# Optimization experiments

Hardware: AMD Instinct MI355X
Metric: run time of the kernel (lower is better)

Reference implementation:

```python
import jax, jax.numpy as jnp
import numpy as np

LN_EPS = 1e-5

def _layer_norm(x, g, b):
    mu = jnp.mean(x, axis=-1, keepdims=True)
    var = jnp.mean(jnp.square(x - mu), axis=-1, keepdims=True)
    return (x - mu) * jax.lax.rsqrt(var + LN_EPS) * g + b

def setup_inputs() -> dict:
    key = jax.random.key(0)
    ks = jax.random.split(key, 12)
    B, L, E, H, W = 4, 1024, 1024, 16, 128
    s = 0.02
    return {
        "x": jax.random.normal(ks[0], (B, L, E), dtype=jnp.float32),
        "in_proj_w": jax.random.normal(ks[1], (3 * E, E), dtype=jnp.float32) * s,
        "in_proj_b": jnp.zeros((3 * E,), dtype=jnp.float32),
        "out_proj_w": jax.random.normal(ks[2], (E, E), dtype=jnp.float32) * s,
        "out_proj_b": jnp.zeros((E,), dtype=jnp.float32),
        "ln1_g": jnp.ones((E,), dtype=jnp.float32),
        "ln1_b": jnp.zeros((E,), dtype=jnp.float32),
        "w1": jax.random.normal(ks[3], (4 * E, E), dtype=jnp.float32) * s,
        "b1": jnp.zeros((4 * E,), dtype=jnp.float32),
        "w2": jax.random.normal(ks[4], (E, 4 * E), dtype=jnp.float32) * s,
        "b2": jnp.zeros((E,), dtype=jnp.float32),
        "ln2_g": jnp.ones((E,), dtype=jnp.float32),
        "ln2_b": jnp.zeros((E,), dtype=jnp.float32),
        "n_head": 16,
        "window_size": 128,
    }

def reference(x, in_proj_w, in_proj_b, out_proj_w, out_proj_b,
              ln1_g, ln1_b, w1, b1, w2, b2, ln2_g, ln2_b,
              n_head, window_size):
    B, L, E = x.shape
    H = n_head
    D = E // H
    # qkv projection (torch Linear convention: y = x @ W.T + b)
    qkv = jnp.einsum('ble,fe->blf', x, in_proj_w) + in_proj_b  # [B,L,3E]
    q, k, v = jnp.split(qkv, 3, axis=-1)
    q = q.reshape(B, L, H, D).transpose(0, 2, 1, 3)  # [B,H,L,D]
    k = k.reshape(B, L, H, D).transpose(0, 2, 1, 3)
    v = v.reshape(B, L, H, D).transpose(0, 2, 1, 3)
    scores = jnp.einsum('bhld,bhmd->bhlm', q, k) / np.sqrt(D)  # [B,H,L,L]
    # banded window mask: allowed iff |i-j| <= window_size (same as the double loop)
    idx = jnp.arange(L)
    band = jnp.abs(idx[:, None] - idx[None, :]) <= window_size  # [L,L]
    scores = jnp.where(band[None, None], scores, -jnp.inf)
    attn = jax.nn.softmax(scores, axis=-1)  # [B,H,L,L]
    ctx = jnp.einsum('bhlm,bhmd->bhld', attn, v)  # [B,H,L,D]
    ctx = ctx.transpose(0, 2, 1, 3).reshape(B, L, E)
    attn_out = jnp.einsum('ble,fe->blf', ctx, out_proj_w) + out_proj_b
    attn_weights = jnp.mean(attn, axis=1)  # torch MHA averages heads -> [B,L,L]
    # residual + norm1 (dropout is identity in eval)
    h = _layer_norm(x + attn_out, ln1_g, ln1_b)
    # positionwise FFN
    ff = jnp.einsum('ble,fe->blf', h, w1) + b1
    ff = jax.nn.relu(ff)
    ff = jnp.einsum('blf,ef->ble', ff, w2) + b2
    out = _layer_norm(h + ff, ln2_g, ln2_b)
    return (out, attn_weights)
```

## Files before the change

### kernel.cpp

```cpp
#include <hip/hip_runtime.h>

#define BB 4
#define LL 1024
#define EE 1024
#define HH 16
#define DD 64

typedef __attribute__((ext_vector_type(8))) short short8;
typedef __attribute__((ext_vector_type(4))) float floatx4;

#define PSTR ((size_t)4096 * 1024)

__device__ __forceinline__ float bf2f(short s) {
    union { unsigned u; float f; } c;
    c.u = ((unsigned)(unsigned short)s) << 16;
    return c.f;
}
__device__ __forceinline__ short f2bf(float f) {
    union { float f; unsigned u; } c; c.f = f;
    unsigned r = c.u + 0x7fffu + ((c.u >> 16) & 1u);
    return (short)(r >> 16);
}

__device__ __forceinline__ void async_copy16(const void* g, void* l) {
    __builtin_amdgcn_global_load_lds(
        (const __attribute__((address_space(1))) unsigned int*)g,
        (__attribute__((address_space(3))) unsigned int*)l, 16, 0, 0);
}

__global__ __launch_bounds__(256) void cvt5(
    const float* __restrict__ x, const float* __restrict__ wqkv,
    const float* __restrict__ wo, const float* __restrict__ w1,
    const float* __restrict__ w2,
    short* __restrict__ xb, short* __restrict__ wqkvb, short* __restrict__ wob,
    short* __restrict__ w1b, short* __restrict__ w2b)
{
    int bi = blockIdx.x;
    const float* in; short* out; int base;
    if      (bi <  4096) { in = x;    out = xb;    base = 0;     }
    else if (bi <  7168) { in = wqkv; out = wqkvb; base = 4096;  }
    else if (bi <  8192) { in = wo;   out = wob;   base = 7168;  }
    else if (bi < 12288) { in = w1;   out = w1b;   base = 8192;  }
    else                 { in = w2;   out = w2b;   base = 12288; }
    int i = (bi - base) * 256 + threadIdx.x;
    float4 v = ((const float4*)in)[i];
    unsigned long long u =
          (unsigned long long)(unsigned short)f2bf(v.x)
        | ((unsigned long long)(unsigned short)f2bf(v.y) << 16)
        | ((unsigned long long)(unsigned short)f2bf(v.z) << 32)
        | ((unsigned long long)(unsigned short)f2bf(v.w) << 48);
    ((unsigned long long*)out)[i] = u;
}

template<bool RELU, bool SK>
__global__ __launch_bounds__(512, 2) void gemm256(
    const short* __restrict__ A, const short* __restrict__ Bw,
    const float* __restrict__ bias,
    short* __restrict__ Cb,
    int M, int N, int K, int Ksp)
{
    __shared__ short SH[67584];
    const int tid  = threadIdx.x;
    const int w    = tid >> 6, lane = tid & 63;
    const int fr   = lane & 15, quad = lane >> 4;
    const int wm   = w >> 2,  wn   = w & 3;

    const int gx   = gridDim.x;
    const int flat = blockIdx.y * gx + blockIdx.x;
    const int nwg  = gx * gridDim.y;
    const int q8   = nwg >> 3;
    const int swz  = (flat & 7) * q8 + (flat >> 3);
    const int m0   = (swz % gx) * 256;
    const int n0   = (swz / gx) * 256;

    const int kb = SK ? blockIdx.z * Ksp : 0;
    const int NT = (SK ? Ksp : K) >> 5;

    auto stageA = [&](int s) {
        if (s >= NT) return;
#pragma unroll
        for (int l = 0; l < 2; ++l) {
            int r = l * 128 + (tid >> 2);
            int g = (tid & 3) ^ ((r >> 1) & 3);
            async_copy16(A + (size_t)(m0 + r) * K + kb + s * 32 + g * 8,
                         SH + (s & 3) * 16384 + l * 4096 + w * 512);
        }
    };
    auto stageB = [&](int s) {
        if (s >= NT) return;
#pragma unroll
        for (int l = 0; l < 2; ++l) {
            int r = l * 128 + (tid >> 2);
            int g = (tid & 3) ^ ((r >> 1) & 3);
            async_copy16(Bw + (size_t)(n0 + r) * K + kb + s * 32 + g * 8,
                         SH + (s & 3) * 16384 + 8192 + l * 4096 + w * 512);
        }
    };

    floatx4 acc[8][4];
#pragma unroll
    for (int i = 0; i < 8; ++i)
#pragma unroll
        for (int j = 0; j < 4; ++j) acc[i][j] = (floatx4){0.f, 0.f, 0.f, 0.f};

    stageA(0); stageB(0); stageA(1); stageB(1); stageA(2); stageB(2);

    const int pos = (quad ^ ((fr >> 1) & 3)) * 8;

    for (int t = 0; t < NT; ++t) {
        if (t + 2 < NT)      asm volatile("s_waitcnt vmcnt(8)" ::: "memory");
        else if (t + 1 < NT) asm volatile("s_waitcnt vmcnt(4)" ::: "memory");
        else                 asm volatile("s_waitcnt vmcnt(0)" ::: "memory");
        __builtin_amdgcn_sched_barrier(0);
        __builtin_amdgcn_s_barrier();
        __builtin_amdgcn_sched_barrier(0);

        const short* sA = SH + (t & 3) * 16384;
        const short* sB = sA + 8192;

        stageA(t + 3);

        short8 af[8], bf[4];
#pragma unroll
        for (int i = 0; i < 4; ++i) af[i] = *(const short8*)&sA[(wm * 128 + i * 16 + fr) * 32 + pos];
#pragma unroll
        for (int j = 0; j < 4; ++j) bf[j] = *(const short8*)&sB[(wn * 64 + j * 16 + fr) * 32 + pos];

        __builtin_amdgcn_s_setprio(1);
#pragma unroll
        for (int i = 0; i < 4; ++i)
#pragma unroll
            for (int j = 0; j < 4; ++j)
                acc[i][j] = __builtin_amdgcn_mfma_f32_16x16x32_bf16(af[i], bf[j], acc[i][j], 0, 0, 0);
        __builtin_amdgcn_s_setprio(0);

        stageB(t + 3);
#pragma unroll
        for (int i = 0; i < 4; ++i) af[i + 4] = *(const short8*)&sA[(wm * 128 + (i + 4) * 16 + fr) * 32 + pos];

        __builtin_amdgcn_s_setprio(1);
#pragma unroll
        for (int i = 0; i < 4; ++i)
#pragma unroll
            for (int j = 0; j < 4; ++j)
                acc[i + 4][j] = __builtin_amdgcn_mfma_f32_16x16x32_bf16(af[i + 4], bf[j], acc[i + 4][j], 0, 0, 0);
        __builtin_amdgcn_s_setprio(0);
        __builtin_amdgcn_sched_barrier(0);
    }

    __syncthreads();

    const int cc = lane & 15, rb4 = quad * 4;
#pragma unroll
    for (int i = 0; i < 8; ++i) {
        int row = wm * 128 + i * 16 + rb4;
#pragma unroll
        for (int j = 0; j < 4; ++j) {
            int col = wn * 64 + j * 16 + cc;
            float bv = SK ? 0.0f : bias[n0 + col];
#pragma unroll
            for (int r = 0; r < 4; ++r) {
                float v = acc[i][j][r] + bv;
                if (RELU) v = fmaxf(v, 0.0f);
                SH[(row + r) * 264 + col] = f2bf(v);
            }
        }
    }
    __syncthreads();
    short* Co = Cb + (SK ? (size_t)blockIdx.z * PSTR : 0);
#pragma unroll
    for (int it = 0; it < 16; ++it) {
        int idx = it * 512 + tid;
        int row = idx >> 5, ch = idx & 31;
        short8 v = *(const short8*)&SH[row * 264 + ch * 8];
        *(short8*)&Co[(size_t)(m0 + row) * N + n0 + ch * 8] = v;
    }
}

__global__ __launch_bounds__(256) void vtrans(const short* __restrict__ qkv,
                                              short* __restrict__ vt)
{
    int id = blockIdx.x;
    int tb = id & 15, h = (id >> 4) & 15, b = id >> 8;
    __shared__ short T[64 * 72];
    const short* src = qkv + (size_t)(b * 1024 + tb * 64) * 3072 + 2048 + h * 64;
    int tok = threadIdx.x >> 2;
    int c8  = threadIdx.x & 3;
#pragma unroll
    for (int q = 0; q < 2; ++q) {
        int d0 = (c8 * 2 + q) * 8;
        short8 v = *(const short8*)&src[(size_t)tok * 3072 + d0];
#pragma unroll
        for (int e = 0; e < 8; ++e) T[(d0 + e) * 72 + tok] = v[e];
    }
    __syncthreads();
    short* dst = vt + (size_t)((b * 16 + h) * 64) * 1024 + tb * 64;
    int d = threadIdx.x >> 2, cq = threadIdx.x & 3;
#pragma unroll
    for (int q = 0; q < 2; ++q) {
        int t0 = (cq * 2 + q) * 8;
        *(short8*)&dst[(size_t)d * 1024 + t0] = *(const short8*)&T[d * 72 + t0];
    }
}

template<bool RELU, bool SK>
__global__ __launch_bounds__(256) void gemm_bt(
    const short* __restrict__ A, const short* __restrict__ Bw,
    const float* __restrict__ bias,
    short* __restrict__ Cb,
    int M, int N, int K, int Ksp)
{
    __shared__ union U {
        struct { short As[128 * 64]; short Bs[128 * 64]; } s;
        short Cs[128 * 136];
    } u;
    const int tid  = threadIdx.x;
    const int wave = tid >> 6, lane = tid & 63;
    const int m0 = blockIdx.x * 128, n0 = blockIdx.y * 128;
    const int wm = (wave & 1) * 64, wn = (wave >> 1) * 64;
    const int kbase = SK ? blockIdx.z * Ksp : 0;

    floatx4 acc[4][4];
#pragma unroll
    for (int i = 0; i < 4; ++i)
#pragma unroll
        for (int j = 0; j < 4; ++j) acc[i][j] = (floatx4){0.f, 0.f, 0.f, 0.f};

    const int srow = wave * 8 + (lane >> 3);
    const int scol = (((lane & 7) ^ ((lane >> 3) & 7))) * 8;
    const short* gA = A  + (size_t)(m0 + srow) * K + kbase + scol;
    const short* gB = Bw + (size_t)(n0 + srow) * K + kbase + scol;
    short* lA = u.s.As + wave * 512;
    short* lB = u.s.Bs + wave * 512;

    const int fr = lane & 15, quad = lane >> 4;
    const int kiters = (SK ? Ksp : K) >> 6;
    for (int kt = 0; kt < kiters; ++kt) {
#pragma unroll
        for (int s = 0; s < 4; ++s) {
            async_copy16(gA + (size_t)s * 32 * K, lA + s * 2048);
            async_copy16(gB + (size_t)s * 32 * K, lB + s * 2048);
        }
        gA += 64; gB += 64;
        __syncthreads();
#pragma unroll
        for (int ks = 0; ks < 2; ++ks) {
            short8 af[4], bf[4];
#pragma unroll
            for (int i = 0; i < 4; ++i) {
                int pos = ((ks * 4 + quad) ^ (fr & 7)) * 8;
                af[i] = *(const short8*)&u.s.As[(wm + i * 16 + fr) * 64 + pos];
                bf[i] = *(const short8*)&u.s.Bs[(wn + i * 16 + fr) * 64 + pos];
            }
#pragma unroll
            for (int i = 0; i < 4; ++i)
#pragma unroll
                for (int j = 0; j < 4; ++j)
                    acc[i][j] = __builtin_amdgcn_mfma_f32_16x16x32_bf16(af[i], bf[j], acc[i][j], 0, 0, 0);
        }
        __syncthreads();
    }

    const int cc = lane & 15;
    const int rb = (lane >> 4) * 4;
#pragma unroll
    for (int j = 0; j < 4; ++j) {
        int col = wn + j * 16 + cc;
        float bv = SK ? 0.0f : bias[n0 + col];
#pragma unroll
        for (int i = 0; i < 4; ++i) {
            int row = wm + i * 16 + rb;
#pragma unroll
            for (int r = 0; r < 4; ++r) {
                float v = acc[i][j][r] + bv;
                if (RELU) v = fmaxf(v, 0.0f);
                u.Cs[(row + r) * 136 + col] = f2bf(v);
            }
        }
    }
    __syncthreads();
    short* Co = Cb + (SK ? (size_t)blockIdx.z * PSTR : 0);
    const int trow = tid >> 4, tcol = (tid & 15) * 8;
#pragma unroll
    for (int p = 0; p < 8; ++p) {
        int row = p * 16 + trow;
        short8 vv = *(const short8*)&u.Cs[row * 136 + tcol];
        *(short8*)&Co[(size_t)(m0 + row) * N + n0 + tcol] = vv;
    }
}

__global__ __launch_bounds__(256) void ln_kernel(
    const float* __restrict__ xa, const short* __restrict__ parts, int nparts,
    const float* __restrict__ bias,
    const float* __restrict__ g, const float* __restrict__ beta,
    float* __restrict__ outf, short* __restrict__ outb)
{
    const int row = blockIdx.x;
    const int tid = threadIdx.x;
    float4 va = ((const float4*)(xa + (size_t)row * EE))[tid];
    float4 vb = ((const float4*)bias)[tid];
    float v0 = va.x + vb.x, v1 = va.y + vb.y, v2 = va.z + vb.z, v3 = va.w + vb.w;
#pragma unroll 4
    for (int p = 0; p < nparts; ++p) {
        unsigned long long u8 = ((const unsigned long long*)(parts + p * PSTR + (size_t)row * EE))[tid];
        v0 += bf2f((short)(u8 & 0xffff));
        v1 += bf2f((short)((u8 >> 16) & 0xffff));
        v2 += bf2f((short)((u8 >> 32) & 0xffff));
        v3 += bf2f((short)(u8 >> 48));
    }
    float s  = v0 + v1 + v2 + v3;
    float ss = v0 * v0 + v1 * v1 + v2 * v2 + v3 * v3;
#pragma unroll
    for (int o = 1; o < 64; o <<= 1) { s += __shfl_xor(s, o); ss += __shfl_xor(ss, o); }
    __shared__ float red[8];
    if ((tid & 63) == 0) { red[(tid >> 6) * 2] = s; red[(tid >> 6) * 2 + 1] = ss; }
    __syncthreads();
    s  = red[0] + red[2] + red[4] + red[6];
    ss = red[1] + red[3] + red[5] + red[7];
    float mean = s * (1.0f / EE);
    float var  = ss * (1.0f / EE) - mean * mean;
    float rstd = rsqrtf(var + 1e-5f);
    float4 vg = ((const float4*)g)[tid];
    float4 vt = ((const float4*)beta)[tid];
    float o0 = (v0 - mean) * rstd * vg.x + vt.x;
    float o1 = (v1 - mean) * rstd * vg.y + vt.y;
    float o2 = (v2 - mean) * rstd * vg.z + vt.z;
    float o3 = (v3 - mean) * rstd * vg.w + vt.w;
    if (outf) ((float4*)(outf + (size_t)row * EE))[tid] = make_float4(o0, o1, o2, o3);
    if (outb) {
        unsigned long long u =
              (unsigned long long)(unsigned short)f2bf(o0)
            | ((unsigned long long)(unsigned short)f2bf(o1) << 16)
            | ((unsigned long long)(unsigned short)f2bf(o2) << 32)
            | ((unsigned long long)(unsigned short)f2bf(o3) << 48);
        ((unsigned long long*)(outb + (size_t)row * EE))[tid] = u;
    }
}

__global__ __launch_bounds__(512, 4) void attn_mfma(
    const short* __restrict__ qkv,
    const short* __restrict__ vt,
    short* __restrict__ ctxp,
    short* __restrict__ pb)
{
    __shared__ short Kl[64 * 320];
    __shared__ float Red[2][2][64];
    const int tid = threadIdx.x, w = tid >> 6, lane = tid & 63;
    const int quad = lane >> 4, mcol = lane & 15;
    const int id = blockIdx.x;
    const int i0 = (id >> 6) * 64, h = id & 15, b = (id >> 4) & 3;
    const int jb0 = i0 - 128;

    const short* qb = qkv + (size_t)(b * 1024) * 3072 + h * 64;
    const short* kb = qb + 1024;

    {
        short* dstb = Kl + w * 512;
#pragma unroll
        for (int it = 0; it < 5; ++it) {
            int jo = it * 64 + w * 8 + (lane >> 3);
            int j  = min(max(jb0 + jo, 0), 1023);
            int g  = (lane & 7) ^ (jo & 7);
            async_copy16(kb + (size_t)j * 3072 + g * 8, dstb + it * 4096);
        }
    }

    const int mt = w >> 1, qtr = w & 1;
    const short* qrow = qb + (size_t)(i0 + mt * 16 + mcol) * 3072 + quad * 8;
    short8 aq0 = *(const short8*)qrow;
    short8 aq1 = *(const short8*)(qrow + 32);

    __syncthreads();

    floatx4 sacc[10];
#pragma unroll
    for (int c = 0; c < 10; ++c) sacc[c] = (floatx4){0.f, 0.f, 0.f, 0.f};
#pragma unroll
    for (int c = 0; c < 10; ++c) {
        int jo = qtr * 160 + c * 16 + mcol;
        const short* krow = Kl + jo * 64;
        short8 b0 = *(const short8*)&krow[((quad    ) ^ (jo & 7)) * 8];
        short8 b1 = *(const short8*)&krow[((4 + quad) ^ (jo & 7)) * 8];
        sacc[c] = __builtin_amdgcn_mfma_f32_16x16x32_bf16(aq0, b0, sacc[c], 0, 0, 0);
        sacc[c] = __builtin_amdgcn_mfma_f32_16x16x32_bf16(aq1, b1, sacc[c], 0, 0, 0);
    }

    const int row0 = mt * 16 + quad * 4;
#pragma unroll
    for (int r = 0; r < 4; ++r) {
        int row = row0 + r;
        float m = -1e30f;
#pragma unroll
        for (int c = 0; c < 10; ++c) {
            int jo = qtr * 160 + c * 16 + mcol;
            bool val = (jo >= row) && (jo <= row + 256) && ((unsigned)(jb0 + jo) < 1024u);
            float s = val ? sacc[c][r] * 0.125f : -1e30f;
            sacc[c][r] = s;
            m = fmaxf(m, s);
        }
        m = fmaxf(m, __shfl_xor(m, 1));
        m = fmaxf(m, __shfl_xor(m, 2));
        m = fmaxf(m, __shfl_xor(m, 4));
        m = fmaxf(m, __shfl_xor(m, 8));
        if (mcol == 0) Red[qtr][0][row] = m;
    }
    __syncthreads();
#pragma unroll
    for (int r = 0; r < 4; ++r) {
        int row = row0 + r;
        float M = fmaxf(Red[0][0][row], Red[1][0][row]);
        float l = 0.f;
#pragma unroll
        for (int c = 0; c < 10; ++c) {
            float p = __expf(sacc[c][r] - M);
            sacc[c][r] = p;
            l += p;
        }
        l += __shfl_xor(l, 1);
        l += __shfl_xor(l, 2);
        l += __shfl_xor(l, 4);
        l += __shfl_xor(l, 8);
        if (mcol == 0) Red[qtr][1][row] = l;
    }
    __syncthreads();
    short* Pl = Kl;
#pragma unroll
    for (int r = 0; r < 4; ++r) {
        int row = row0 + r;
        float inv = 1.0f / (Red[0][1][row] + Red[1][1][row]);
#pragma unroll
        for (int c = 0; c < 10; ++c) {
            int jo = qtr * 160 + c * 16 + mcol;
            Pl[row * 320 + (((jo >> 3) ^ (row & 7)) * 8) + (jo & 7)] = f2bf(sacc[c][r] * inv);
        }
    }
    __syncthreads();

    const int pmt = w & 3, dth = w >> 2;
    floatx4 cacc[2];
    cacc[0] = (floatx4){0.f, 0.f, 0.f, 0.f};
    cacc[1] = (floatx4){0.f, 0.f, 0.f, 0.f};
    const int prow = (pmt * 16 + mcol) * 320;
    const short* vb0 = vt + ((size_t)((b * 16 + h) * 64 + dth * 32) + mcol) * 1024;
#pragma unroll
    for (int jc = 0; jc < 10; ++jc) {
        short8 ap = *(const short8*)&Pl[prow + (((jc * 4 + quad) ^ (mcol & 7)) * 8)];
        int jg = jb0 + jc * 32 + quad * 8;
        if ((unsigned)jg >= 1024u) jg = 0;
        short8 bv0 = *(const short8*)(vb0 + jg);
        short8 bv1 = *(const short8*)(vb0 + (size_t)16 * 1024 + jg);
        cacc[0] = __builtin_amdgcn_mfma_f32_16x16x32_bf16(ap, bv0, cacc[0], 0, 0, 0);
        cacc[1] = __builtin_amdgcn_mfma_f32_16x16x32_bf16(ap, bv1, cacc[1], 0, 0, 0);
    }

    short* pbb = pb + ((size_t)((b * 16 + h) * 1024) + i0) * 320;
#pragma unroll
    for (int s = 0; s < 5; ++s) {
        int t = s * 512 + tid;
        int row = t / 40, c = t - row * 40;
        short8 v = *(const short8*)&Pl[row * 320 + ((c ^ (row & 7)) * 8)];
        *(short8*)&pbb[(size_t)t * 8] = v;
    }
    __syncthreads();

    short* Ct = Kl;
#pragma unroll
    for (int d2 = 0; d2 < 2; ++d2)
#pragma unroll
        for (int r = 0; r < 4; ++r)
            Ct[(pmt * 16 + quad * 4 + r) * 72 + dth * 32 + d2 * 16 + mcol] = f2bf(cacc[d2][r]);
    __syncthreads();
    short* cb = ctxp + (size_t)(b * 1024 + i0) * 1024 + h * 64;
    {
        int row = tid >> 3, c = tid & 7;
        short8 v = *(const short8*)&Ct[row * 72 + c * 8];
        *(short8*)&cb[(size_t)row * 1024 + c * 8] = v;
    }
}

__global__ __launch_bounds__(256) void pb_reduce(const short* __restrict__ pb,
                                                 float* __restrict__ aw)
{
    const int i = blockIdx.x & 1023, b = blockIdx.x >> 10;
    const int i0 = i & ~63;
    __shared__ short P[16 * 320];
    for (int t = threadIdx.x; t < 640; t += 256) {
        int hh = t / 40, c = t - hh * 40;
        ((short8*)P)[t] = *(const short8*)(pb +
            ((size_t)((b * 16 + hh) * 1024) + i) * 320 + c * 8);
    }
    __syncthreads();
    float* row = aw + ((size_t)(b * 1024) + i) * 1024;
    for (int j = threadIdx.x; j < 1024; j += 256) {
        int jo = j - i0 + 128;
        float s = 0.f;
        if ((unsigned)jo < 320u) {
#pragma unroll
            for (int hh = 0; hh < 16; ++hh)
                s += bf2f(P[hh * 320 + jo]);
            s *= (1.0f / 16.0f);
        }
        row[j] = s;
    }
}

extern "C" void kernel_launch(void* const* d_in, const int* in_sizes, int n_in,
                              void* d_out, int out_size, void* d_ws, size_t ws_size,
                              hipStream_t stream) {
    const float* x    = (const float*)d_in[0];
    const float* wqkv = (const float*)d_in[1];
    const float* bqkv = (const float*)d_in[2];
    const float* wo   = (const float*)d_in[3];
    const float* bo   = (const float*)d_in[4];
    const float* g1   = (const float*)d_in[5];
    const float* be1  = (const float*)d_in[6];
    const float* w1   = (const float*)d_in[7];
    const float* bb1  = (const float*)d_in[8];
    const float* w2   = (const float*)d_in[9];
    const float* bb2  = (const float*)d_in[10];
    const float* g2   = (const float*)d_in[11];
    const float* be2  = (const float*)d_in[12];

    char* ws = (char*)d_ws;
    size_t off = 0;
    auto take = [&](size_t bytes) {
        void* p = ws + off;
        off += (bytes + 255) & ~(size_t)255;
        return p;
    };
    short* xb     = (short*)take((size_t)4096 * 1024 * 2);
    short* wqkv_b = (short*)take((size_t)3072 * 1024 * 2);
    short* wo_b   = (short*)take((size_t)1024 * 1024 * 2);
    short* w1_b   = (short*)take((size_t)4096 * 1024 * 2);
    short* w2_b   = (short*)take((size_t)1024 * 4096 * 2);
    short* qkv_b  = (short*)take((size_t)4096 * 3072 * 2);
    short* ctx_b  = (short*)take((size_t)4096 * 1024 * 2);
    short* ff2_p  = qkv_b;
    short* attn_p = (short*)take((size_t)2 * 4096 * 1024 * 2);
    float* h_f    = (float*)take((size_t)4096 * 1024 * 4);
    short* vt_ws  = (short*)h_f;
    short* h_b    = (short*)take((size_t)4096 * 1024 * 2);
    short* pb_ws  = (short*)take((size_t)4 * 16 * 1024 * 320 * 2);
    short* ff_b   = pb_ws;

    float* out_f = (float*)d_out;
    float* attnW = (float*)d_out + (size_t)4 * 1024 * 1024;

    cvt5<<<16384, 256, 0, stream>>>(x, wqkv, wo, w1, w2, xb, wqkv_b, wo_b, w1_b, w2_b);

    gemm256<false, false><<<dim3(16, 12), 512, 0, stream>>>(
        xb, wqkv_b, bqkv, qkv_b, 4096, 3072, 1024, 1024);

    vtrans<<<1024, 256, 0, stream>>>(qkv_b, vt_ws);

    attn_mfma<<<1024, 512, 0, stream>>>(qkv_b, vt_ws, ctx_b, pb_ws);

    pb_reduce<<<4096, 256, 0, stream>>>(pb_ws, attnW);

    gemm_bt<false, true><<<dim3(32, 8, 2), 256, 0, stream>>>(
        ctx_b, wo_b, nullptr, attn_p, 4096, 1024, 1024, 512);

    ln_kernel<<<4096, 256, 0, stream>>>(x, attn_p, 2, bo, g1, be1, h_f, h_b);

    gemm256<true, false><<<dim3(16, 16), 512, 0, stream>>>(
        h_b, w1_b, bb1, ff_b, 4096, 4096, 1024, 1024);

    gemm256<false, true><<<dim3(16, 4, 4), 512, 0, stream>>>(
        ff_b, w2_b, nullptr, ff2_p, 4096, 1024, 4096, 1024);

    ln_kernel<<<4096, 256, 0, stream>>>(h_f, ff2_p, 4, bb2, g2, be2, out_f, nullptr);
}
```

Before: 332.9 us.

## Switch GEMM mainloop to K=64 tiles with two-stage double buffering

The bf16 MFMA GEMM mainloop now processes 64-wide K tiles instead of 32, using two LDS buffers with a single `__syncthreads` per step in place of a four-stage ring with hand-tuned `vmcnt` waits. The A and B staging are merged into one lambda with an 8-way XOR swizzle suited to the wider rows, and each iteration issues two K-halves of 32 MFMAs. This halves the number of barriers per K and lets more MFMAs run per sync. The trade-off is that prefetch depth drops from three tiles ahead to one, so global-load latency may be hidden less well.

```diff
diff --git a/kernel.cpp b/kernel.cpp
--- a/kernel.cpp
+++ b/kernel.cpp
@@ -74,28 +74,27 @@
     const int n0   = (swz / gx) * 256;
 
     const int kb = SK ? blockIdx.z * Ksp : 0;
-    const int NT = (SK ? Ksp : K) >> 5;
-
-    auto stageA = [&](int s) {
+    const int NT = (SK ? Ksp : K) >> 6;
+
+    const int srow = w * 8 + (lane >> 3);
+    const int sg   = lane & 7;
+    auto stage = [&](int s) {
         if (s >= NT) return;
 #pragma unroll
-        for (int l = 0; l < 2; ++l) {
-            int r = l * 128 + (tid >> 2);
-            int g = (tid & 3) ^ ((r >> 1) & 3);
-            async_copy16(A + (size_t)(m0 + r) * K + kb + s * 32 + g * 8,
-                         SH + (s & 3) * 16384 + l * 4096 + w * 512);
+        for (int i = 0; i < 4; ++i) {
+            int r = i * 64 + srow;
+            int g = sg ^ (r & 7);
+            async_copy16(A + (size_t)(m0 + r) * K + kb + s * 64 + g * 8,
+                         SH + (s & 1) * 32768 + i * 4096 + w * 512);
+        }
+#pragma unroll
+        for (int i = 0; i < 4; ++i) {
+            int r = i * 64 + srow;
+            int g = sg ^ (r & 7);
+            async_copy16(Bw + (size_t)(n0 + r) * K + kb + s * 64 + g * 8,
+                         SH + (s & 1) * 32768 + 16384 + i * 4096 + w * 512);
         }
     };
-    auto stageB = [&](int s) {
-        if (s >= NT) return;
-#pragma unroll
-        for (int l = 0; l < 2; ++l) {
-            int r = l * 128 + (tid >> 2);
-            int g = (tid & 3) ^ ((r >> 1) & 3);
-            async_copy16(Bw + (size_t)(n0 + r) * K + kb + s * 32 + g * 8,
-                         SH + (s & 3) * 16384 + 8192 + l * 4096 + w * 512);
-        }
-    };
 
     floatx4 acc[8][4];
 #pragma unroll
@@ -103,49 +102,45 @@
 #pragma unroll
         for (int j = 0; j < 4; ++j) acc[i][j] = (floatx4){0.f, 0.f, 0.f, 0.f};
 
-    stageA(0); stageB(0); stageA(1); stageB(1); stageA(2); stageB(2);
-
-    const int pos = (quad ^ ((fr >> 1) & 3)) * 8;
+    stage(0);
+
+    const int posk0 = ((quad    ) ^ (fr & 7)) * 8;
+    const int posk1 = ((4 + quad) ^ (fr & 7)) * 8;
 
     for (int t = 0; t < NT; ++t) {
-        if (t + 2 < NT)      asm volatile("s_waitcnt vmcnt(8)" ::: "memory");
-        else if (t + 1 < NT) asm volatile("s_waitcnt vmcnt(4)" ::: "memory");
-        else                 asm volatile("s_waitcnt vmcnt(0)" ::: "memory");
+        __syncthreads();
         __builtin_amdgcn_sched_barrier(0);
-        __builtin_amdgcn_s_barrier();
-        __builtin_amdgcn_sched_barrier(0);
-
-        const short* sA = SH + (t & 3) * 16384;
-        const short* sB = sA + 8192;
-
-        stageA(t + 3);
-
-        short8 af[8], bf[4];
-#pragma unroll
-        for (int i = 0; i < 4; ++i) af[i] = *(const short8*)&sA[(wm * 128 + i * 16 + fr) * 32 + pos];
-#pragma unroll
-        for (int j = 0; j < 4; ++j) bf[j] = *(const short8*)&sB[(wn * 64 + j * 16 + fr) * 32 + pos];
-
+
+        const short* sA = SH + (t & 1) * 32768;
+        const short* sB = sA + 16384;
+
+        stage(t + 1);
+
+        short8 a0[8], b0[4];
+#pragma unroll
+        for (int i = 0; i < 8; ++i) a0[i] = *(const short8*)&sA[(wm * 128 + i * 16 + fr) * 64 + posk0];
+#pragma unroll
+        for (int j = 0; j < 4; ++j) b0[j] = *(const short8*)&sB[(wn * 64 + j * 16 + fr) * 64 + posk0];
         __builtin_amdgcn_s_setprio(1);
 #pragma unroll
-        for (int i = 0; i < 4; ++i)
+        for (int i = 0; i < 8; ++i)
 #pragma unroll
             for (int j = 0; j < 4; ++j)
-                acc[i][j] = __builtin_amdgcn_mfma_f32_16x16x32_bf16(af[i], bf[j], acc[i][j], 0, 0, 0);
+                acc[i][j] = __builtin_amdgcn_mfma_f32_16x16x32_bf16(a0[i], b0[j], acc[i][j], 0, 0, 0);
         __builtin_amdgcn_s_setprio(0);
 
-        stageB(t + 3);
-#pragma unroll
-        for (int i = 0; i < 4; ++i) af[i + 4] = *(const short8*)&sA[(wm * 128 + (i + 4) * 16 + fr) * 32 + pos];
-
+        short8 a1[8], b1[4];
+#pragma unroll
+        for (int i = 0; i < 8; ++i) a1[i] = *(const short8*)&sA[(wm * 128 + i * 16 + fr) * 64 + posk1];
+#pragma unroll
+        for (int j = 0; j < 4; ++j) b1[j] = *(const short8*)&sB[(wn * 64 + j * 16 + fr) * 64 + posk1];
         __builtin_amdgcn_s_setprio(1);
 #pragma unroll
-        for (int i = 0; i < 4; ++i)
+        for (int i = 0; i < 8; ++i)
 #pragma unroll
             for (int j = 0; j < 4; ++j)
-                acc[i + 4][j] = __builtin_amdgcn_mfma_f32_16x16x32_bf16(af[i + 4], bf[j], acc[i + 4][j], 0, 0, 0);
+                acc[i][j] = __builtin_amdgcn_mfma_f32_16x16x32_bf16(a1[i], b1[j], acc[i][j], 0, 0, 0);
         __builtin_amdgcn_s_setprio(0);
-        __builtin_amdgcn_sched_barrier(0);
     }
 
     __syncthreads();
```

Result: faster. 322.0 us (-3.3%).
